# Kernel tuning notes

Measured on AMD Instinct MI355X. Metric: run time of the kernel, lower is better.

## Reference

```python
import jax, jax.numpy as jnp
import numpy as np

# LinearAdderV1: out[b,o] = sum_i (input[b,i] + weight[o,i]); out *= bias[o]
# The broadcast-add-then-reduce is mathematically separable:
#   sum_i (x[b,i] + w[o,i]) = sum_i x[b,i] + sum_i w[o,i]
# so we compute it without materializing the (B, O, I) intermediate. Same math,
# identical up to fp summation order.

B = 4096
IN = 4096
OUT = 4096


def setup_inputs() -> dict:
    key = jax.random.key(0)
    k1, k2, k3 = jax.random.split(key, 3)
    inp = jax.random.normal(k1, (B, IN), dtype=jnp.float32)
    # kaiming_uniform-ish scale for weight, uniform bias in [-1/sqrt(fan_in), +)
    bound_w = float(np.sqrt(6.0 / ((1.0 + 5.0) * IN)))  # a=sqrt(5) => gain^2=2/(1+5)
    weight = jax.random.uniform(k2, (OUT, IN), dtype=jnp.float32, minval=-bound_w, maxval=bound_w)
    bound_b = float(1.0 / np.sqrt(IN))
    bias_param = jax.random.uniform(k3, (OUT,), dtype=jnp.float32, minval=-bound_b, maxval=bound_b)
    return {"input": inp, "weight": weight, "bias_param": bias_param}


def reference(input, weight, bias_param):
    # (B, 1) + (1, OUT) -> (B, OUT)
    x_sum = jnp.sum(input, axis=-1, keepdims=True)          # (B, 1)
    w_sum = jnp.sum(weight, axis=-1)                        # (OUT,)
    out = x_sum + w_sum[None, :]                            # (B, OUT)
    out = out * bias_param[None, :]
    return out
```

## Files before the change

### kernel.cpp

```cpp
#include <hip/hip_runtime.h>

#define B_DIM   4096
#define IN_DIM  4096
#define OUT_DIM 4096

typedef float floatx4 __attribute__((ext_vector_type(4)));

__global__ __launch_bounds__(256) void wsum_kernel(
    const float* __restrict__ weight, const float* __restrict__ bias,
    float* __restrict__ wb)
{
    const int wave = threadIdx.x >> 6;
    const int lane = threadIdx.x & 63;
    const int o    = blockIdx.x * 4 + wave;

    const floatx4* src4 = (const floatx4*)(weight + (size_t)o * IN_DIM);

    float s0 = 0.f, s1 = 0.f, s2 = 0.f, s3 = 0.f;
    #pragma unroll
    for (int k = 0; k < 16; k += 4) {
        floatx4 v0 = __builtin_nontemporal_load(&src4[lane + (k + 0) * 64]);
        floatx4 v1 = __builtin_nontemporal_load(&src4[lane + (k + 1) * 64]);
        floatx4 v2 = __builtin_nontemporal_load(&src4[lane + (k + 2) * 64]);
        floatx4 v3 = __builtin_nontemporal_load(&src4[lane + (k + 3) * 64]);
        s0 += (v0.x + v0.y) + (v0.z + v0.w);
        s1 += (v1.x + v1.y) + (v1.z + v1.w);
        s2 += (v2.x + v2.y) + (v2.z + v2.w);
        s3 += (v3.x + v3.y) + (v3.z + v3.w);
    }
    float s = (s0 + s1) + (s2 + s3);

    #pragma unroll
    for (int off = 32; off > 0; off >>= 1)
        s += __shfl_down(s, off, 64);

    if (lane == 0)
        wb[o] = s * bias[o];
}

__global__ __launch_bounds__(256) void fused_kernel(
    const float* __restrict__ input, const float* __restrict__ bias,
    const float* __restrict__ wb, float* __restrict__ out)
{
    const int b = blockIdx.x;
    const int t = threadIdx.x;

    const floatx4* in4 = (const floatx4*)(input + (size_t)b * IN_DIM);

    floatx4 v[4];
    #pragma unroll
    for (int k = 0; k < 4; ++k)
        v[k] = __builtin_nontemporal_load(&in4[t + k * 256]);

    float s = 0.f;
    #pragma unroll
    for (int k = 0; k < 4; ++k)
        s += (v[k].x + v[k].y) + (v[k].z + v[k].w);

    #pragma unroll
    for (int off = 32; off > 0; off >>= 1)
        s += __shfl_down(s, off, 64);

    __shared__ float sm[4];
    if ((t & 63) == 0) sm[t >> 6] = s;
    __syncthreads();
    const float xs = (sm[0] + sm[1]) + (sm[2] + sm[3]);

    const floatx4* bias4 = (const floatx4*)bias;
    const floatx4* wb4   = (const floatx4*)wb;
    floatx4* out4 = (floatx4*)out + (size_t)b * (OUT_DIM / 4);

    #pragma unroll
    for (int k = 0; k < 4; ++k) {
        const int i = t + k * 256;
        const floatx4 bi = bias4[i];
        const floatx4 w  = wb4[i];
        floatx4 r;
        r.x = fmaf(xs, bi.x, w.x);
        r.y = fmaf(xs, bi.y, w.y);
        r.z = fmaf(xs, bi.z, w.z);
        r.w = fmaf(xs, bi.w, w.w);
        __builtin_nontemporal_store(r, &out4[i]);
    }
}

extern "C" void kernel_launch(void* const* d_in, const int* in_sizes, int n_in,
                              void* d_out, int out_size, void* d_ws, size_t ws_size,
                              hipStream_t stream) {
    const float* input  = (const float*)d_in[0];
    const float* weight = (const float*)d_in[1];
    const float* bias   = (const float*)d_in[2];
    float* out = (float*)d_out;
    float* wb  = (float*)d_ws;

    wsum_kernel<<<OUT_DIM / 4, 256, 0, stream>>>(weight, bias, wb);
    fused_kernel<<<B_DIM, 256, 0, stream>>>(input, bias, wb, out);
}
```

Baseline: 163.9 us.

## Compute input and weight row sums in one kernel, then write output separately

Moves the input row reductions out of the output kernel into the same launch as the weight row sums, so both reductions share one grid of 2048 blocks. The output kernel now only reads the precomputed row sums and writes four output rows per block, reusing the bias and weight-sum loads across those rows. This splits the read-heavy and write-heavy phases into separate kernels. The cost is an extra small workspace round trip and the loss of overlap between input reads and output writes that the fused kernel had.

```diff
diff --git a/kernel.cpp b/kernel.cpp
--- a/kernel.cpp
+++ b/kernel.cpp
@@ -6,15 +6,18 @@
 
 typedef float floatx4 __attribute__((ext_vector_type(4)));
 
-__global__ __launch_bounds__(256) void wsum_kernel(
-    const float* __restrict__ weight, const float* __restrict__ bias,
-    float* __restrict__ wb)
+__global__ __launch_bounds__(256) void sums_kernel(
+    const float* __restrict__ input, const float* __restrict__ weight,
+    const float* __restrict__ bias, float* __restrict__ wb,
+    float* __restrict__ xs)
 {
     const int wave = threadIdx.x >> 6;
     const int lane = threadIdx.x & 63;
-    const int o    = blockIdx.x * 4 + wave;
+    const bool is_w = (blockIdx.x < (OUT_DIM / 4));
+    const int row  = (is_w ? blockIdx.x : (blockIdx.x - OUT_DIM / 4)) * 4 + wave;
+    const float* __restrict__ base = is_w ? weight : input;
 
-    const floatx4* src4 = (const floatx4*)(weight + (size_t)o * IN_DIM);
+    const floatx4* src4 = (const floatx4*)(base + (size_t)row * IN_DIM);
 
     float s0 = 0.f, s1 = 0.f, s2 = 0.f, s3 = 0.f;
     #pragma unroll
@@ -34,53 +37,46 @@
     for (int off = 32; off > 0; off >>= 1)
         s += __shfl_down(s, off, 64);
 
-    if (lane == 0)
-        wb[o] = s * bias[o];
+    if (lane == 0) {
+        if (is_w) wb[row] = s * bias[row];
+        else      xs[row] = s;
+    }
 }
 
-__global__ __launch_bounds__(256) void fused_kernel(
-    const float* __restrict__ input, const float* __restrict__ bias,
-    const float* __restrict__ wb, float* __restrict__ out)
+__global__ __launch_bounds__(256) void write_kernel(
+    const float* __restrict__ bias, const float* __restrict__ wb,
+    const float* __restrict__ xs, float* __restrict__ out)
 {
-    const int b = blockIdx.x;
-    const int t = threadIdx.x;
+    const int t  = threadIdx.x;
+    const int b0 = blockIdx.x * 4;
 
-    const floatx4* in4 = (const floatx4*)(input + (size_t)b * IN_DIM);
-
-    floatx4 v[4];
-    #pragma unroll
-    for (int k = 0; k < 4; ++k)
-        v[k] = __builtin_nontemporal_load(&in4[t + k * 256]);
-
-    float s = 0.f;
-    #pragma unroll
-    for (int k = 0; k < 4; ++k)
-        s += (v[k].x + v[k].y) + (v[k].z + v[k].w);
-
-    #pragma unroll
-    for (int off = 32; off > 0; off >>= 1)
-        s += __shfl_down(s, off, 64);
-
-    __shared__ float sm[4];
-    if ((t & 63) == 0) sm[t >> 6] = s;
-    __syncthreads();
-    const float xs = (sm[0] + sm[1]) + (sm[2] + sm[3]);
+    const float x0 = xs[b0 + 0];
+    const float x1 = xs[b0 + 1];
+    const float x2 = xs[b0 + 2];
+    const float x3 = xs[b0 + 3];
 
     const floatx4* bias4 = (const floatx4*)bias;
     const floatx4* wb4   = (const floatx4*)wb;
-    floatx4* out4 = (floatx4*)out + (size_t)b * (OUT_DIM / 4);
+    floatx4* out4 = (floatx4*)out;
 
     #pragma unroll
     for (int k = 0; k < 4; ++k) {
         const int i = t + k * 256;
         const floatx4 bi = bias4[i];
         const floatx4 w  = wb4[i];
-        floatx4 r;
-        r.x = fmaf(xs, bi.x, w.x);
-        r.y = fmaf(xs, bi.y, w.y);
-        r.z = fmaf(xs, bi.z, w.z);
-        r.w = fmaf(xs, bi.w, w.w);
-        __builtin_nontemporal_store(r, &out4[i]);
+        floatx4 r0, r1, r2, r3;
+        r0.x = fmaf(x0, bi.x, w.x); r0.y = fmaf(x0, bi.y, w.y);
+        r0.z = fmaf(x0, bi.z, w.z); r0.w = fmaf(x0, bi.w, w.w);
+        r1.x = fmaf(x1, bi.x, w.x); r1.y = fmaf(x1, bi.y, w.y);
+        r1.z = fmaf(x1, bi.z, w.z); r1.w = fmaf(x1, bi.w, w.w);
+        r2.x = fmaf(x2, bi.x, w.x); r2.y = fmaf(x2, bi.y, w.y);
+        r2.z = fmaf(x2, bi.z, w.z); r2.w = fmaf(x2, bi.w, w.w);
+        r3.x = fmaf(x3, bi.x, w.x); r3.y = fmaf(x3, bi.y, w.y);
+        r3.z = fmaf(x3, bi.z, w.z); r3.w = fmaf(x3, bi.w, w.w);
+        __builtin_nontemporal_store(r0, &out4[(size_t)(b0 + 0) * (OUT_DIM / 4) + i]);
+        __builtin_nontemporal_store(r1, &out4[(size_t)(b0 + 1) * (OUT_DIM / 4) + i]);
+        __builtin_nontemporal_store(r2, &out4[(size_t)(b0 + 2) * (OUT_DIM / 4) + i]);
+        __builtin_nontemporal_store(r3, &out4[(size_t)(b0 + 3) * (OUT_DIM / 4) + i]);
     }
 }
 
@@ -92,7 +88,8 @@
     const float* bias   = (const float*)d_in[2];
     float* out = (float*)d_out;
     float* wb  = (float*)d_ws;
+    float* xs  = (float*)d_ws + OUT_DIM;
 
-    wsum_kernel<<<OUT_DIM / 4, 256, 0, stream>>>(weight, bias, wb);
-    fused_kernel<<<B_DIM, 256, 0, stream>>>(input, bias, wb, out);
+    sums_kernel<<<2 * (OUT_DIM / 4), 256, 0, stream>>>(input, weight, bias, wb, xs);
+    write_kernel<<<B_DIM / 4, 256, 0, stream>>>(bias, wb, xs, out);
 }
```

New measurement: 160.5 us. -2.1%, faster.
